# Kernel tuning notes

Hardware: AMD Instinct MI355X
Metric: run time of the kernel (lower is better)

The kernel has to match this reference:

```python
import jax, jax.numpy as jnp
import numpy as np

T, B, C, H, L = 512, 64, 256, 1024, 2


def setup_inputs() -> dict:
    key = jax.random.key(0)
    ks = jax.random.split(key, 12)
    s_c = 1.0 / np.sqrt(C)
    s_h = 1.0 / np.sqrt(H)
    return {
        "x": jax.random.normal(ks[0], (T, B, C), jnp.float32),
        "h0": jnp.zeros((L, B, H), jnp.float32),
        # layer 0 (input size C)
        "w_ih0": jax.random.uniform(ks[1], (H, C), jnp.float32, -s_h, s_h),
        "w_hh0": jax.random.uniform(ks[2], (H, H), jnp.float32, -s_h, s_h),
        "b_ih0": jax.random.uniform(ks[3], (H,), jnp.float32, -s_h, s_h),
        "b_hh0": jax.random.uniform(ks[4], (H,), jnp.float32, -s_h, s_h),
        # layer 1 (input size H)
        "w_ih1": jax.random.uniform(ks[5], (H, H), jnp.float32, -s_h, s_h),
        "w_hh1": jax.random.uniform(ks[6], (H, H), jnp.float32, -s_h, s_h),
        "b_ih1": jax.random.uniform(ks[7], (H,), jnp.float32, -s_h, s_h),
        "b_hh1": jax.random.uniform(ks[8], (H,), jnp.float32, -s_h, s_h),
        # decoder Linear(H -> C)
        "w_dec": jax.random.uniform(ks[9], (C, H), jnp.float32, -s_h, s_h),
        "b_dec": jax.random.uniform(ks[10], (C,), jnp.float32, -s_h, s_h),
    }


def _rnn_layer(x, h0, w_ih, w_hh, b_ih, b_hh):
    # Precompute the input projection for all timesteps (one big GEMM),
    # then scan the sequential tanh recurrence: h_t = tanh(x_t W_ih^T + b_ih + h_{t-1} W_hh^T + b_hh)
    xw = jnp.einsum("tbi,hi->tbh", x, w_ih) + b_ih + b_hh  # [T, B, H]

    def step(h, xt):
        h = jnp.tanh(xt + h @ w_hh.T)
        return h, h

    h_last, ys = jax.lax.scan(step, h0, xw)
    return ys, h_last


def reference(x, h0, w_ih0, w_hh0, b_ih0, b_hh0, w_ih1, w_hh1, b_ih1, b_hh1, w_dec, b_dec):
    y0, h_last0 = _rnn_layer(x, h0[0], w_ih0, w_hh0, b_ih0, b_hh0)
    y1, h_last1 = _rnn_layer(y0, h0[1], w_ih1, w_hh1, b_ih1, b_hh1)
    decoded = jnp.einsum("tbh,ch->tbc", y1, w_dec) + b_dec  # [T, B, C]
    hidden = jnp.stack([h_last0, h_last1], axis=0)  # [L, B, H]
    return decoded, hidden
```

## Files before the change

### kernel.cpp

```cpp
#include <hip/hip_runtime.h>

#define T_STEPS 512
#define BB 64
#define CC 256
#define HH 1024
#define TBROWS (T_STEPS*BB)
#define BH (BB*HH)
#define FLSTRIDE 32
#define FPS (8*32*FLSTRIDE)

typedef unsigned short u16;
typedef _Float16 f16;
typedef f16 f16x8 __attribute__((ext_vector_type(8)));
typedef float f32x4 __attribute__((ext_vector_type(4)));
typedef unsigned int u32x4 __attribute__((ext_vector_type(4)));
typedef unsigned int u32x2 __attribute__((ext_vector_type(2)));

__device__ __forceinline__ f32x4 mfma16h(f16x8 a, f16x8 b, f32x4 c) {
  return __builtin_amdgcn_mfma_f32_16x16x32_f16(a, b, c, 0, 0, 0);
}
__device__ __forceinline__ u16 f2h_bits(float f) {
  return __builtin_bit_cast(unsigned short, (f16)f);
}

__global__ void sentinel_kernel(float* o, float v) { o[0] = v; }

__global__ __launch_bounds__(256) void cvt_h(const float* __restrict__ src,
                                             u16* __restrict__ dst, int n4) {
  int i = blockIdx.x * 256 + threadIdx.x;
  if (i >= n4) return;
  const float4 v = ((const float4*)src)[i];
  float vv[4] = {v.x, v.y, v.z, v.w};
  uint2 o;
  o.x = (unsigned)f2h_bits(vv[0]) | ((unsigned)f2h_bits(vv[1]) << 16);
  o.y = (unsigned)f2h_bits(vv[2]) | ((unsigned)f2h_bits(vv[3]) << 16);
  ((uint2*)dst)[i] = o;
}

__global__ __launch_bounds__(256) void add_bias_kernel(const float* __restrict__ a,
                                                       const float* __restrict__ b,
                                                       float* __restrict__ o, int n) {
  int i = blockIdx.x * 256 + threadIdx.x;
  if (i < n) o[i] = a[i] + b[i];
}

__global__ __launch_bounds__(256) void gemmh(const u16* __restrict__ Ah,
                                             const u16* __restrict__ Wh,
                                             const float* __restrict__ bias,
                                             float* __restrict__ Cd,
                                             int M, int N, int K) {
  __shared__ u16 As[128][48];
  __shared__ u16 Bs[128][48];
  const int tid = threadIdx.x;
  const int nblk = N >> 7;
  const int mb = blockIdx.x / nblk;
  const int nb = blockIdx.x % nblk;
  const int m0 = mb << 7, n0 = nb << 7;
  const int lane = tid & 63, wave = tid >> 6;
  const int wm = (wave >> 1) * 64, wn = (wave & 1) * 64;
  const int fr = lane & 15, kg = lane >> 4;

  f32x4 acc[4][4];
#pragma unroll
  for (int i = 0; i < 4; ++i)
#pragma unroll
    for (int j = 0; j < 4; ++j) acc[i][j] = (f32x4){0.f, 0.f, 0.f, 0.f};

  const int sr = tid >> 1;
  const int sk = (tid & 1) * 16;

  for (int k0 = 0; k0 < K; k0 += 32) {
    __syncthreads();
    const size_t aoff = (size_t)(m0 + sr) * K + k0 + sk;
    *(uint4*)&As[sr][sk]     = *(const uint4*)(Ah + aoff);
    *(uint4*)&As[sr][sk + 8] = *(const uint4*)(Ah + aoff + 8);
    const size_t woff = (size_t)(n0 + sr) * K + k0 + sk;
    *(uint4*)&Bs[sr][sk]     = *(const uint4*)(Wh + woff);
    *(uint4*)&Bs[sr][sk + 8] = *(const uint4*)(Wh + woff + 8);
    __syncthreads();

    f16x8 ah[4], bh[4];
#pragma unroll
    for (int i = 0; i < 4; ++i) {
      ah[i] = *(const f16x8*)&As[wm + i * 16 + fr][kg * 8];
      bh[i] = *(const f16x8*)&Bs[wn + i * 16 + fr][kg * 8];
    }
#pragma unroll
    for (int i = 0; i < 4; ++i)
#pragma unroll
      for (int j = 0; j < 4; ++j)
        acc[i][j] = mfma16h(ah[i], bh[j], acc[i][j]);
  }

#pragma unroll
  for (int j = 0; j < 4; ++j) {
    const int n = n0 + wn + j * 16 + fr;
    const float bv = bias ? bias[n] : 0.f;
#pragma unroll
    for (int i = 0; i < 4; ++i) {
#pragma unroll
      for (int r = 0; r < 4; ++r) {
        const int m = m0 + wm + i * 16 + kg * 4 + r;
        Cd[(size_t)m * N + n] = acc[i][j][r] + bv;
      }
    }
  }
}


__device__ __forceinline__ int claim_role(int* claim, int* role_s, int tid) {
  if (tid == 0) {
    int xcd;
    asm volatile("s_getreg_b32 %0, hwreg(20, 0, 32)" : "=s"(xcd));
    xcd &= 7;
    int slot = __hip_atomic_fetch_add(claim + xcd * 32, 1, __ATOMIC_RELAXED,
                                      __HIP_MEMORY_SCOPE_AGENT) & 31;
    *role_s = xcd * 32 + slot;
  }
  __syncthreads();
  return *role_s;
}

__device__ __forceinline__ void poll_n(const int* base, int nf, int lane) {
  const int* p = base + (size_t)(lane & (nf - 1)) * FLSTRIDE;
  while (true) {
    int v = (lane < nf) ? __hip_atomic_load(p, __ATOMIC_RELAXED, __HIP_MEMORY_SCOPE_AGENT) : 1;
    if (__all(v != 0)) break;
    __builtin_amdgcn_s_sleep(1);
  }
}

__global__ __launch_bounds__(1024) void rnn_scanA(
    const u16* __restrict__ Wh,
    const u16* __restrict__ cin, u16* __restrict__ cout,
    const float* __restrict__ xw,
    u16* __restrict__ y0,
    float* __restrict__ hlast,
    int* __restrict__ flags, int* __restrict__ claim, int nsteps) {
  __shared__ u16 Ws[32][1024];
  __shared__ f32x4 red[2][2][7][64];
  __shared__ int role_s, pcnt;

  const int tid = threadIdx.x;
  const int lane = tid & 63, wave = tid >> 6;
  const int c2 = wave & 1, q = wave >> 1;
  const int fr = lane & 15, kg = lane >> 4;

  if (tid == 2) pcnt = 0;
  const int role = claim_role(claim, &role_s, tid);
  const int xcd = role >> 5, slot = role & 31;
  const int n0 = slot << 5;
  const int bb = (xcd << 3) + (fr & 7);

  auto wsp = [&](int r, int cbyte) -> u16* {
    return (u16*)((char*)Ws + (size_t)r * 2048 + (cbyte ^ ((r & 7) << 4)));
  };
  {
#pragma unroll
    for (int j = 0; j < 4; ++j) {
      const int off = tid * 64 + j * 16;
      const int row = off >> 11;
      const int cbyte = off & 2047;
      const u16* src = Wh + (size_t)(n0 + row) * HH + (cbyte >> 1);
      *(uint4*)wsp(row, cbyte) = *(const uint4*)src;
    }
  }
  __syncthreads();

  const int co = n0 + c2 * 16 + (kg << 2);
  const size_t hoff = (size_t)bb * HH + q * 128 + (kg << 3);
  const int wrow = c2 * 16 + fr;

  for (int t = 0; t < nsteps; ++t) {
    const size_t obase = (size_t)t * BH;
    float4 xwv;
    if (q == 0 && fr < 8) xwv = *(const float4*)(xw + obase + (size_t)bb * HH + co);

    if (t > 0)
      poll_n(flags + (((size_t)(t - 1) * 8 + xcd) * 32 + q * 4) * FLSTRIDE, 4, lane);
    __atomic_signal_fence(__ATOMIC_ACQUIRE);

    const u16* pb = ((t == 0) ? cin : (y0 + (size_t)(t - 1) * BH)) + hoff;

    u32x4 hv[4];
#pragma unroll
    for (int kc = 0; kc < 4; ++kc)
      asm volatile("global_load_dwordx4 %0, %1, off offset:%2"
                   : "=v"(hv[kc]) : "v"(pb), "i"(kc * 64));
    asm volatile("s_waitcnt vmcnt(0)" ::: "memory");
    __builtin_amdgcn_sched_barrier(0);

    f32x4 acc0 = (f32x4){0.f, 0.f, 0.f, 0.f}, acc1 = acc0;
#pragma unroll
    for (int kc = 0; kc < 4; ++kc) {
      f16x8 hb = __builtin_bit_cast(f16x8, hv[kc]);
      const int cb = q * 256 + kc * 64 + kg * 16;
      f16x8 wh = *(const f16x8*)wsp(wrow, cb);
      if (kc & 1) acc1 = mfma16h(wh, hb, acc1); else acc0 = mfma16h(wh, hb, acc0);
    }
    f32x4 accv = acc0 + acc1;

    if (q != 0) red[t & 1][c2][q - 1][lane] = accv;
    __syncthreads();

    if (q == 0) {
#pragma unroll
      for (int i = 0; i < 7; ++i) accv += red[t & 1][c2][i][lane];
      float hvv[4]; u16 qb[4];
#pragma unroll
      for (int r = 0; r < 4; ++r) {
        hvv[r] = tanhf(accv[r] + ((const float*)&xwv)[r]);
        qb[r] = f2h_bits(hvv[r]);
      }
      if (fr < 8) {
        const size_t oi = obase + (size_t)bb * HH + co;
        u32x2 hp;
        hp.x = (unsigned)qb[0] | ((unsigned)qb[1] << 16);
        hp.y = (unsigned)qb[2] | ((unsigned)qb[3] << 16);
        *(u32x2*)(y0 + oi) = hp;
        if (t == nsteps - 1) {
          *(u32x2*)(cout + (size_t)bb * HH + co) = hp;
          *(float4*)(hlast + (size_t)bb * HH + co) = (float4){hvv[0], hvv[1], hvv[2], hvv[3]};
        }
      }
      asm volatile("s_waitcnt vmcnt(0)" ::: "memory");
      if (lane == 0) {
        int old = __hip_atomic_fetch_add(&pcnt, 1, __ATOMIC_ACQ_REL, __HIP_MEMORY_SCOPE_WORKGROUP);
        if (old & 1) {
          int* fp = flags + (((size_t)t * 8 + xcd) * 32 + slot) * FLSTRIDE;
          __hip_atomic_store(fp, 1, __ATOMIC_RELAXED, __HIP_MEMORY_SCOPE_AGENT);
        }
      }
    }
  }
}

__global__ __launch_bounds__(1024) void rnn_scanB(
    const u16* __restrict__ Wih, const u16* __restrict__ Whh,
    const u16* __restrict__ cin, u16* __restrict__ cout,
    const float* __restrict__ b1,
    const u16* __restrict__ y0,
    u16* __restrict__ y1,
    float* __restrict__ hlast,
    int* __restrict__ flags, int* __restrict__ claim, int nsteps) {
  __shared__ u16 Ws[32][2048];
  __shared__ f32x4 red[2][2][7][64];
  __shared__ int role_s, pcnt;

  const int tid = threadIdx.x;
  const int lane = tid & 63, wave = tid >> 6;
  const int c2 = wave & 1, q = wave >> 1;
  const int fr = lane & 15, kg = lane >> 4;

  if (tid == 2) pcnt = 0;
  const int role = claim_role(claim, &role_s, tid);
  const int xcd = role >> 5, slot = role & 31;
  const int n0 = slot << 5;
  const int bb = (xcd << 3) + (fr & 7);

  auto wsp = [&](int r, int cbyte) -> u16* {
    return (u16*)((char*)Ws + (size_t)r * 4096 + (cbyte ^ ((r & 7) << 4)));
  };
  {
#pragma unroll
    for (int j = 0; j < 8; ++j) {
      const int off = tid * 128 + j * 16;
      const int row = off >> 12;
      const int cbyte = off & 4095;
      const int k = cbyte >> 1;
      const u16* src = (k < 1024) ? (Wih + (size_t)(n0 + row) * HH + k)
                                  : (Whh + (size_t)(n0 + row) * HH + (k - 1024));
      *(uint4*)wsp(row, cbyte) = *(const uint4*)src;
    }
  }
  __syncthreads();

  const int co = n0 + c2 * 16 + (kg << 2);
  const size_t hoff = (size_t)bb * HH + ((q < 4) ? q * 256 : (q - 4) * 256) + (kg << 3);
  const int wrow = c2 * 16 + fr;
  float4 b1v;
  if (q == 0 && fr < 8) b1v = *(const float4*)(b1 + co);

  for (int t = 0; t < nsteps; ++t) {
    const size_t obase = (size_t)t * BH;

    if (t > 0 && q >= 4)
      poll_n(flags + (((size_t)(t - 1) * 8 + xcd) * 32 + (q - 4) * 8) * FLSTRIDE, 8, lane);
    __atomic_signal_fence(__ATOMIC_ACQUIRE);

    const u16* pb = (q < 4) ? (y0 + obase + hoff)
                            : (((t == 0) ? cin : (y1 + (size_t)(t - 1) * BH)) + hoff);

    u32x4 hv[8];
#pragma unroll
    for (int kc = 0; kc < 8; ++kc)
      asm volatile("global_load_dwordx4 %0, %1, off offset:%2"
                   : "=v"(hv[kc]) : "v"(pb), "i"(kc * 64));
    asm volatile("s_waitcnt vmcnt(0)" ::: "memory");
    __builtin_amdgcn_sched_barrier(0);

    f32x4 acc0 = (f32x4){0.f, 0.f, 0.f, 0.f}, acc1 = acc0;
#pragma unroll
    for (int kc = 0; kc < 8; ++kc) {
      f16x8 hb = __builtin_bit_cast(f16x8, hv[kc]);
      const int cb = q * 512 + kc * 64 + kg * 16;
      f16x8 wh = *(const f16x8*)wsp(wrow, cb);
      if (kc & 1) acc1 = mfma16h(wh, hb, acc1); else acc0 = mfma16h(wh, hb, acc0);
    }
    f32x4 accv = acc0 + acc1;

    if (q != 0) red[t & 1][c2][q - 1][lane] = accv;
    __syncthreads();

    if (q == 0) {
#pragma unroll
      for (int i = 0; i < 7; ++i) accv += red[t & 1][c2][i][lane];
      float hvv[4]; u16 qb[4];
#pragma unroll
      for (int r = 0; r < 4; ++r) {
        hvv[r] = tanhf(accv[r] + ((const float*)&b1v)[r]);
        qb[r] = f2h_bits(hvv[r]);
      }
      if (fr < 8) {
        const size_t oi = obase + (size_t)bb * HH + co;
        u32x2 hp;
        hp.x = (unsigned)qb[0] | ((unsigned)qb[1] << 16);
        hp.y = (unsigned)qb[2] | ((unsigned)qb[3] << 16);
        *(u32x2*)(y1 + oi) = hp;
        if (t == nsteps - 1) {
          *(u32x2*)(cout + (size_t)bb * HH + co) = hp;
          *(float4*)(hlast + (size_t)bb * HH + co) = (float4){hvv[0], hvv[1], hvv[2], hvv[3]};
        }
      }
      asm volatile("s_waitcnt vmcnt(0)" ::: "memory");
      if (lane == 0) {
        int old = __hip_atomic_fetch_add(&pcnt, 1, __ATOMIC_ACQ_REL, __HIP_MEMORY_SCOPE_WORKGROUP);
        if (old & 1) {
          int* fp = flags + (((size_t)t * 8 + xcd) * 32 + slot) * FLSTRIDE;
          __hip_atomic_store(fp, 1, __ATOMIC_RELAXED, __HIP_MEMORY_SCOPE_AGENT);
        }
      }
    }
  }
}

struct Ptrs {
  u16 *wih0_h, *whh0_h, *wih1_h, *whh1_h, *wdec_h;
  float *b0, *b1;
  u16 *carA, *carB;
  int* flags;
  int* claim;
  u16 *x_h;
  float* xw;
  u16 *y0, *y1;
  size_t total;
};

static Ptrs make_plan(char* base, int CT) {
  Ptrs p;
  size_t off = 0;
  auto take = [&](size_t bytes) -> char* {
    off = (off + 255) & ~(size_t)255;
    char* q = base + off;
    off += bytes;
    return q;
  };
  p.wih0_h  = (u16*)take((size_t)HH * CC * 2);
  p.whh0_h  = (u16*)take((size_t)HH * HH * 2);
  p.wih1_h  = (u16*)take((size_t)HH * HH * 2);
  p.whh1_h  = (u16*)take((size_t)HH * HH * 2);
  p.wdec_h  = (u16*)take((size_t)CC * HH * 2);
  p.b0      = (float*)take((size_t)HH * 4);
  p.b1      = (float*)take((size_t)HH * 4);
  p.carA    = (u16*)take((size_t)2 * BH * 2);
  p.carB    = (u16*)take((size_t)2 * BH * 2);
  p.flags   = (int*)take((size_t)2 * T_STEPS * FPS * 4);
  p.claim   = (int*)take((size_t)128 * 8 * 32 * 4);
  p.x_h     = (u16*)take((size_t)CT * BB * CC * 2);
  p.xw      = (float*)take((size_t)CT * BH * 4);
  p.y0      = (u16*)take((size_t)CT * BH * 2);
  p.y1      = (u16*)take((size_t)CT * BH * 2);
  p.total   = off;
  return p;
}

extern "C" void kernel_launch(void* const* d_in, const int* in_sizes, int n_in,
                              void* d_out, int out_size, void* d_ws, size_t ws_size,
                              hipStream_t stream) {
  (void)in_sizes; (void)n_in; (void)out_size;
  const float* x     = (const float*)d_in[0];
  const float* h0    = (const float*)d_in[1];
  const float* w_ih0 = (const float*)d_in[2];
  const float* w_hh0 = (const float*)d_in[3];
  const float* b_ih0 = (const float*)d_in[4];
  const float* b_hh0 = (const float*)d_in[5];
  const float* w_ih1 = (const float*)d_in[6];
  const float* w_hh1 = (const float*)d_in[7];
  const float* b_ih1 = (const float*)d_in[8];
  const float* b_hh1 = (const float*)d_in[9];
  const float* w_dec = (const float*)d_in[10];
  const float* b_dec = (const float*)d_in[11];
  float* out = (float*)d_out;

  int CT = T_STEPS;
  Ptrs P = make_plan((char*)d_ws, CT);
  while (P.total > ws_size && CT > 8) {
    CT >>= 1;
    P = make_plan((char*)d_ws, CT);
  }
  if (P.total > ws_size) {
    sentinel_kernel<<<1, 1, 0, stream>>>(out, (float)ws_size);
    return;
  }
  const int NCH = T_STEPS / CT;

  (void)hipMemsetAsync(P.flags, 0, (size_t)2 * T_STEPS * FPS * 4, stream);
  (void)hipMemsetAsync(P.claim, 0, (size_t)128 * 8 * 32 * 4, stream);

  cvt_h<<<HH * CC / 1024, 256, 0, stream>>>(w_ih0, P.wih0_h, HH * CC / 4);
  cvt_h<<<HH * HH / 1024, 256, 0, stream>>>(w_hh0, P.whh0_h, HH * HH / 4);
  cvt_h<<<HH * HH / 1024, 256, 0, stream>>>(w_ih1, P.wih1_h, HH * HH / 4);
  cvt_h<<<HH * HH / 1024, 256, 0, stream>>>(w_hh1, P.whh1_h, HH * HH / 4);
  cvt_h<<<CC * HH / 1024, 256, 0, stream>>>(w_dec, P.wdec_h, CC * HH / 4);
  cvt_h<<<2 * BH / 1024, 256, 0, stream>>>(h0, P.carA, 2 * BH / 4);
  add_bias_kernel<<<HH / 256, 256, 0, stream>>>(b_ih0, b_hh0, P.b0, HH);
  add_bias_kernel<<<HH / 256, 256, 0, stream>>>(b_ih1, b_hh1, P.b1, HH);

  float* hlast0 = out + (size_t)TBROWS * CC;
  float* hlast1 = hlast0 + BH;

  for (int c = 0; c < NCH; ++c) {
    const int t0 = c * CT;
    const u16* cin = (c & 1) ? P.carB : P.carA;
    u16* cout = (c & 1) ? P.carA : P.carB;

    cvt_h<<<CT * BB * CC / 1024, 256, 0, stream>>>(x + (size_t)t0 * BB * CC, P.x_h,
                                                   CT * BB * CC / 4);
    gemmh<<<(CT * BB / 128) * (HH / 128), 256, 0, stream>>>(P.x_h, P.wih0_h, P.b0, P.xw,
                                                            CT * BB, HH, CC);
    rnn_scanA<<<256, 1024, 0, stream>>>(
        P.whh0_h, cin, cout, P.xw, P.y0, hlast0,
        P.flags + (size_t)t0 * FPS, P.claim + (size_t)(2 * c) * 256, CT);
    rnn_scanB<<<256, 1024, 0, stream>>>(
        P.wih1_h, P.whh1_h, cin + BH, cout + BH, P.b1, P.y0, P.y1, hlast1,
        P.flags + (size_t)(T_STEPS + t0) * FPS, P.claim + (size_t)(2 * c + 1) * 256, CT);
    gemmh<<<(CT * BB / 128) * (CC / 128), 256, 0, stream>>>(P.y1, P.wdec_h, b_dec,
                                                            out + (size_t)t0 * BB * CC,
                                                            CT * BB, CC, HH);
  }
}
```

Measured before the change: 4.459 ms.

## Hoist layer-1 input projection into a batched GEMM and reuse single-layer scan kernel

Layer 1's input projection y0·W_ih1^T is no longer computed inside the sequential scan. It is now computed once per chunk by a tiled fp16 GEMM into the xw buffer, and layer 1 then reuses the same recurrent-only scan kernel as layer 0. This halves the per-step matmul work and LDS weight footprint on the latency-bound recurrent critical path, moving that work to a throughput-friendly GEMM. In exchange it adds one extra kernel launch per chunk and a full fp32 [CT,B,H] write and read of xw.

```diff
diff --git a/kernel.cpp b/kernel.cpp
--- a/kernel.cpp
+++ b/kernel.cpp
@@ -130,11 +130,11 @@
   }
 }
 
-__global__ __launch_bounds__(1024) void rnn_scanA(
+__global__ __launch_bounds__(1024) void rnn_scan(
     const u16* __restrict__ Wh,
     const u16* __restrict__ cin, u16* __restrict__ cout,
     const float* __restrict__ xw,
-    u16* __restrict__ y0,
+    u16* __restrict__ y,
     float* __restrict__ hlast,
     int* __restrict__ flags, int* __restrict__ claim, int nsteps) {
   __shared__ u16 Ws[32][1024];
@@ -180,7 +180,7 @@
       poll_n(flags + (((size_t)(t - 1) * 8 + xcd) * 32 + q * 4) * FLSTRIDE, 4, lane);
     __atomic_signal_fence(__ATOMIC_ACQUIRE);
 
-    const u16* pb = ((t == 0) ? cin : (y0 + (size_t)(t - 1) * BH)) + hoff;
+    const u16* pb = ((t == 0) ? cin : (y + (size_t)(t - 1) * BH)) + hoff;
 
     u32x4 hv[4];
 #pragma unroll
@@ -217,116 +217,7 @@
         u32x2 hp;
         hp.x = (unsigned)qb[0] | ((unsigned)qb[1] << 16);
         hp.y = (unsigned)qb[2] | ((unsigned)qb[3] << 16);
-        *(u32x2*)(y0 + oi) = hp;
-        if (t == nsteps - 1) {
-          *(u32x2*)(cout + (size_t)bb * HH + co) = hp;
-          *(float4*)(hlast + (size_t)bb * HH + co) = (float4){hvv[0], hvv[1], hvv[2], hvv[3]};
-        }
-      }
-      asm volatile("s_waitcnt vmcnt(0)" ::: "memory");
-      if (lane == 0) {
-        int old = __hip_atomic_fetch_add(&pcnt, 1, __ATOMIC_ACQ_REL, __HIP_MEMORY_SCOPE_WORKGROUP);
-        if (old & 1) {
-          int* fp = flags + (((size_t)t * 8 + xcd) * 32 + slot) * FLSTRIDE;
-          __hip_atomic_store(fp, 1, __ATOMIC_RELAXED, __HIP_MEMORY_SCOPE_AGENT);
-        }
-      }
-    }
-  }
-}
-
-__global__ __launch_bounds__(1024) void rnn_scanB(
-    const u16* __restrict__ Wih, const u16* __restrict__ Whh,
-    const u16* __restrict__ cin, u16* __restrict__ cout,
-    const float* __restrict__ b1,
-    const u16* __restrict__ y0,
-    u16* __restrict__ y1,
-    float* __restrict__ hlast,
-    int* __restrict__ flags, int* __restrict__ claim, int nsteps) {
-  __shared__ u16 Ws[32][2048];
-  __shared__ f32x4 red[2][2][7][64];
-  __shared__ int role_s, pcnt;
-
-  const int tid = threadIdx.x;
-  const int lane = tid & 63, wave = tid >> 6;
-  const int c2 = wave & 1, q = wave >> 1;
-  const int fr = lane & 15, kg = lane >> 4;
-
-  if (tid == 2) pcnt = 0;
-  const int role = claim_role(claim, &role_s, tid);
-  const int xcd = role >> 5, slot = role & 31;
-  const int n0 = slot << 5;
-  const int bb = (xcd << 3) + (fr & 7);
-
-  auto wsp = [&](int r, int cbyte) -> u16* {
-    return (u16*)((char*)Ws + (size_t)r * 4096 + (cbyte ^ ((r & 7) << 4)));
-  };
-  {
-#pragma unroll
-    for (int j = 0; j < 8; ++j) {
-      const int off = tid * 128 + j * 16;
-      const int row = off >> 12;
-      const int cbyte = off & 4095;
-      const int k = cbyte >> 1;
-      const u16* src = (k < 1024) ? (Wih + (size_t)(n0 + row) * HH + k)
-                                  : (Whh + (size_t)(n0 + row) * HH + (k - 1024));
-      *(uint4*)wsp(row, cbyte) = *(const uint4*)src;
-    }
-  }
-  __syncthreads();
-
-  const int co = n0 + c2 * 16 + (kg << 2);
-  const size_t hoff = (size_t)bb * HH + ((q < 4) ? q * 256 : (q - 4) * 256) + (kg << 3);
-  const int wrow = c2 * 16 + fr;
-  float4 b1v;
-  if (q == 0 && fr < 8) b1v = *(const float4*)(b1 + co);
-
-  for (int t = 0; t < nsteps; ++t) {
-    const size_t obase = (size_t)t * BH;
-
-    if (t > 0 && q >= 4)
-      poll_n(flags + (((size_t)(t - 1) * 8 + xcd) * 32 + (q - 4) * 8) * FLSTRIDE, 8, lane);
-    __atomic_signal_fence(__ATOMIC_ACQUIRE);
-
-    const u16* pb = (q < 4) ? (y0 + obase + hoff)
-                            : (((t == 0) ? cin : (y1 + (size_t)(t - 1) * BH)) + hoff);
-
-    u32x4 hv[8];
-#pragma unroll
-    for (int kc = 0; kc < 8; ++kc)
-      asm volatile("global_load_dwordx4 %0, %1, off offset:%2"
-                   : "=v"(hv[kc]) : "v"(pb), "i"(kc * 64));
-    asm volatile("s_waitcnt vmcnt(0)" ::: "memory");
-    __builtin_amdgcn_sched_barrier(0);
-
-    f32x4 acc0 = (f32x4){0.f, 0.f, 0.f, 0.f}, acc1 = acc0;
-#pragma unroll
-    for (int kc = 0; kc < 8; ++kc) {
-      f16x8 hb = __builtin_bit_cast(f16x8, hv[kc]);
-      const int cb = q * 512 + kc * 64 + kg * 16;
-      f16x8 wh = *(const f16x8*)wsp(wrow, cb);
-      if (kc & 1) acc1 = mfma16h(wh, hb, acc1); else acc0 = mfma16h(wh, hb, acc0);
-    }
-    f32x4 accv = acc0 + acc1;
-
-    if (q != 0) red[t & 1][c2][q - 1][lane] = accv;
-    __syncthreads();
-
-    if (q == 0) {
-#pragma unroll
-      for (int i = 0; i < 7; ++i) accv += red[t & 1][c2][i][lane];
-      float hvv[4]; u16 qb[4];
-#pragma unroll
-      for (int r = 0; r < 4; ++r) {
-        hvv[r] = tanhf(accv[r] + ((const float*)&b1v)[r]);
-        qb[r] = f2h_bits(hvv[r]);
-      }
-      if (fr < 8) {
-        const size_t oi = obase + (size_t)bb * HH + co;
-        u32x2 hp;
-        hp.x = (unsigned)qb[0] | ((unsigned)qb[1] << 16);
-        hp.y = (unsigned)qb[2] | ((unsigned)qb[3] << 16);
-        *(u32x2*)(y1 + oi) = hp;
+        *(u32x2*)(y + oi) = hp;
         if (t == nsteps - 1) {
           *(u32x2*)(cout + (size_t)bb * HH + co) = hp;
           *(float4*)(hlast + (size_t)bb * HH + co) = (float4){hvv[0], hvv[1], hvv[2], hvv[3]};
@@ -438,11 +329,13 @@
                                                    CT * BB * CC / 4);
     gemmh<<<(CT * BB / 128) * (HH / 128), 256, 0, stream>>>(P.x_h, P.wih0_h, P.b0, P.xw,
                                                             CT * BB, HH, CC);
-    rnn_scanA<<<256, 1024, 0, stream>>>(
+    rnn_scan<<<256, 1024, 0, stream>>>(
         P.whh0_h, cin, cout, P.xw, P.y0, hlast0,
         P.flags + (size_t)t0 * FPS, P.claim + (size_t)(2 * c) * 256, CT);
-    rnn_scanB<<<256, 1024, 0, stream>>>(
-        P.wih1_h, P.whh1_h, cin + BH, cout + BH, P.b1, P.y0, P.y1, hlast1,
+    gemmh<<<(CT * BB / 128) * (HH / 128), 256, 0, stream>>>(P.y0, P.wih1_h, P.b1, P.xw,
+                                                            CT * BB, HH, HH);
+    rnn_scan<<<256, 1024, 0, stream>>>(
+        P.whh1_h, cin + BH, cout + BH, P.xw, P.y1, hlast1,
         P.flags + (size_t)(T_STEPS + t0) * FPS, P.claim + (size_t)(2 * c + 1) * 256, CT);
     gemmh<<<(CT * BB / 128) * (CC / 128), 256, 0, stream>>>(P.y1, P.wdec_h, b_dec,
                                                             out + (size_t)t0 * BB * CC,
```

New measurement: 3.914 ms. 1.14x faster.
